# Optimization experiments

Hardware: AMD Instinct MI355X
Metric: run time of the kernel (lower is better)

Reference implementation:

```python
import jax, jax.numpy as jnp
import numpy as np

FEATURE_DIM = 1024
MAX_DEPTH = 32
HID = 128
N = 32768


def setup_inputs() -> dict:
    key = jax.random.key(0)
    ks = jax.random.split(key, 16)
    d = FEATURE_DIM
    s = 0.02
    return {
        "features": jax.random.normal(ks[0], (N, d), jnp.float32),
        "depths": jax.random.randint(ks[1], (N,), 0, MAX_DEPTH),
        "pos_emb": jax.random.normal(ks[2], (MAX_DEPTH, d), jnp.float32) * s,
        "aW1": jax.random.normal(ks[3], (HID, 2 * d), jnp.float32) * s,
        "ab1": jnp.zeros((HID,), jnp.float32),
        "aW2": jax.random.normal(ks[4], (1, HID), jnp.float32) * s,
        "ab2": jnp.zeros((1,), jnp.float32),
        "uW1": jax.random.normal(ks[5], (d, 2 * d), jnp.float32) * s,
        "ub1": jnp.zeros((d,), jnp.float32),
        "uW2": jax.random.normal(ks[6], (d, d), jnp.float32) * s,
        "ub2": jnp.zeros((d,), jnp.float32),
        "gW": jax.random.normal(ks[7], (d, 2 * d), jnp.float32) * s,
        "gb": jnp.zeros((d,), jnp.float32),
    }


def reference(features, depths, pos_emb, aW1, ab1, aW2, ab2,
              uW1, ub1, uW2, ub2, gW, gb):
    # add position embeddings (depths clamped to [0, MAX_DEPTH-1])
    dep = jnp.clip(depths, 0, MAX_DEPTH - 1)
    f = features + pos_emb[dep]                       # [N, d]
    target = f[0:1]                                    # [1, d]
    path = f[1:]                                       # [N-1, d]

    # attention MLP over all path states at once (vectorizes the torch loop)
    tb = jnp.broadcast_to(target, path.shape)          # [N-1, d]
    comb = jnp.concatenate([tb, path], axis=1)         # [N-1, 2d]
    h = jax.nn.relu(comb @ aW1.T + ab1)                # [N-1, 128]
    attn = jax.nn.sigmoid(h @ aW2.T + ab2)             # [N-1, 1]

    s = attn.sum()
    attn = jnp.where(s > 0, attn / s, attn)

    agg = (path * attn).sum(axis=0, keepdims=True)     # [1, d]
    c2 = jnp.concatenate([target, agg], axis=1)        # [1, 2d]
    gate = jax.nn.sigmoid(c2 @ gW.T + gb)
    upd = jax.nn.relu(c2 @ uW1.T + ub1) @ uW2.T + ub2
    updated_target = target + gate * upd
    return jnp.concatenate([updated_target, path], axis=0)
```

## Files before the change

kernel.cpp:

```cpp
#include <hip/hip_runtime.h>

#define DNUM 1024
#define HIDN 128
#define NTOT 32768
#define MR 32
#define NBLK 1024

#define T_OFF 0
#define P0_OFF 1024
#define S_OFF 1152
#define AGG_OFF 1216
#define GATE_OFF 2240
#define U1_OFF 3264
#define W2_FOFF 4288
#define AGGP_OFF (W2_FOFF + 65536)
#define SP_OFF (AGGP_OFF + NBLK * DNUM)
#define WS_NEED ((size_t)(SP_OFF + NBLK) * 4)

typedef __attribute__((ext_vector_type(8))) short short8;
typedef __attribute__((ext_vector_type(4))) float f32x4;

__device__ __forceinline__ unsigned short f2bf(float x) {
  unsigned int u = __builtin_bit_cast(unsigned int, x);
  u = u + 0x7fffu + ((u >> 16) & 1u);
  return (unsigned short)(u >> 16);
}
__device__ __forceinline__ float bf2f(unsigned int bits16) {
  unsigned int u = bits16 << 16;
  return __builtin_bit_cast(float, u);
}

__global__ __launch_bounds__(256) void kinit(const float* __restrict__ features,
                                             const int* __restrict__ depths,
                                             const float* __restrict__ pos_emb,
                                             const float* __restrict__ aW1,
                                             const float* __restrict__ ab1,
                                             float* __restrict__ ws,
                                             unsigned short* __restrict__ w2) {
  int t = threadIdx.x, bid = blockIdx.x;
  if (bid == 0) {
    __shared__ float tgt[1024];
    __shared__ float ph[256];
    int dep = depths[0];
    dep = dep < 0 ? 0 : (dep > 31 ? 31 : dep);
    float4 fv = *(const float4*)(features + t * 4);
    float4 pe = *(const float4*)(pos_emb + dep * DNUM + t * 4);
    float4 r;
    r.x = fv.x + pe.x; r.y = fv.y + pe.y; r.z = fv.z + pe.z; r.w = fv.w + pe.w;
    *(float4*)(ws + T_OFF + t * 4) = r;
    *(float4*)(tgt + t * 4) = r;
    if (t < 64) ws[S_OFF + t] = 0.f;
    __syncthreads();
    int j = t >> 1, h = t & 1;
    const float* wrow = aW1 + (size_t)j * (2 * DNUM) + h * 512;
    const float* tr = tgt + h * 512;
    float p = 0.f;
    for (int k = 0; k < 512; k += 4) {
      float4 wv = *(const float4*)(wrow + k);
      float4 tv = *(const float4*)(tr + k);
      p += wv.x * tv.x + wv.y * tv.y + wv.z * tv.z + wv.w * tv.w;
    }
    ph[t] = p;
    __syncthreads();
    if (t < HIDN) ws[P0_OFF + t] = ab1[t] + ph[t * 2] + ph[t * 2 + 1];
    return;
  }
  int idx = ((bid - 1) * 256 + t) * 4;
  int j = idx >> 10, k = idx & 1023;
  float4 v = *(const float4*)(aW1 + (size_t)j * 2048 + 1024 + k);
  uint2 pk;
  pk.x = (unsigned int)f2bf(v.x) | ((unsigned int)f2bf(v.y) << 16);
  pk.y = (unsigned int)f2bf(v.z) | ((unsigned int)f2bf(v.w) << 16);
  *(uint2*)(w2 + idx) = pk;
}

__global__ __launch_bounds__(256) void kstream(const float* __restrict__ features,
                                               const int* __restrict__ depths,
                                               const float* __restrict__ pos_emb,
                                               float* __restrict__ out) {
  const int t = threadIdx.x;
  const int bid = blockIdx.x;
  const int col = t * 4;
#pragma unroll
  for (int rr = 0; rr < 4; ++rr) {
    int fr = 1 + bid * 4 + rr;
    if (fr < NTOT) {
      int dp = depths[fr];
      dp = dp < 0 ? 0 : (dp > 31 ? 31 : dp);
      float4 fv = *(const float4*)(features + (size_t)fr * DNUM + col);
      float4 pe = *(const float4*)(pos_emb + (size_t)dp * DNUM + col);
      float4 f;
      f.x = fv.x + pe.x; f.y = fv.y + pe.y; f.z = fv.z + pe.z; f.w = fv.w + pe.w;
      *(float4*)(out + (size_t)fr * DNUM + col) = f;
    }
  }
}

__global__ __launch_bounds__(512, 4) void kgemm(
    const float* __restrict__ fsrc, const float* __restrict__ p0,
    const float* __restrict__ aW2, const float* __restrict__ ab2,
    const unsigned short* __restrict__ w2,
    float* __restrict__ agg, float* __restrict__ sacc,
    float* __restrict__ aggp, float* __restrict__ sp) {
  __shared__ __align__(16) unsigned char ldsA[MR * 2048];
  __shared__ float part[160];
  __shared__ float comb[1024];
  const int t = threadIdx.x;
  const int bid = blockIdx.x;
  const int lane = t & 63;
  const int w = t >> 6;
  const int llo = lane & 15;
  const int lhi = lane >> 4;
  const int tc = t & 255;
  const int th = t >> 8;
  const int col = tc * 4;

#pragma unroll
  for (int ii = 0; ii < 16; ++ii) {
    int i = ii * 2 + th;
    int fr = 1 + bid * MR + i;
    float4 f = (fr < NTOT) ? *(const float4*)(fsrc + (size_t)fr * DNUM + col)
                           : make_float4(0.f, 0.f, 0.f, 0.f);
    uint2 pk;
    pk.x = (unsigned int)f2bf(f.x) | ((unsigned int)f2bf(f.y) << 16);
    pk.y = (unsigned int)f2bf(f.z) | ((unsigned int)f2bf(f.w) << 16);
    int off = (i * 2048 + tc * 8) ^ ((i & 7) << 4);
    *(uint2*)(ldsA + off) = pk;
  }
  __syncthreads();

  const int wm = w >> 2, wn = w & 3;
  f32x4 acc[2];
  acc[0] = (f32x4){0.f, 0.f, 0.f, 0.f};
  acc[1] = (f32x4){0.f, 0.f, 0.f, 0.f};
  const int arow = wm * 16 + llo;
  const int abase = arow * 2048;
  const int aswz = (arow & 7) << 4;
  const unsigned short* bpA = w2 + (size_t)(wn * 32 + llo) * DNUM + lhi * 8;
  const unsigned short* bpB = bpA + 16 * DNUM;

#pragma unroll 4
  for (int kc = 0; kc < 32; ++kc) {
    int kbase = kc * 32;
    short8 av = *(short8*)(ldsA + ((abase + (kbase + lhi * 8) * 2) ^ aswz));
    short8 bv0 = *(const short8*)(bpA + kbase);
    short8 bv1 = *(const short8*)(bpB + kbase);
    acc[0] = __builtin_amdgcn_mfma_f32_16x16x32_bf16(av, bv0, acc[0], 0, 0, 0);
    acc[1] = __builtin_amdgcn_mfma_f32_16x16x32_bf16(av, bv1, acc[1], 0, 0, 0);
  }

  float p0v[2], wv[2];
#pragma unroll
  for (int n = 0; n < 2; ++n) {
    int j = wn * 32 + n * 16 + llo;
    p0v[n] = p0[j];
    wv[n] = aW2[j];
  }
#pragma unroll
  for (int e = 0; e < 4; ++e) {
    float s = 0.f;
#pragma unroll
    for (int n = 0; n < 2; ++n) {
      float h = acc[n][e] + p0v[n];
      h = fmaxf(h, 0.f);
      s += h * wv[n];
    }
    s += __shfl_xor(s, 1);
    s += __shfl_xor(s, 2);
    s += __shfl_xor(s, 4);
    s += __shfl_xor(s, 8);
    if (llo == 0) part[wn * 32 + wm * 16 + lhi * 4 + e] = s;
  }
  __syncthreads();

  if (t < MR) {
    float pre = part[t] + part[32 + t] + part[64 + t] + part[96 + t] + ab2[0];
    int fr = 1 + bid * MR + t;
    float raw = 0.f;
    if (fr < NTOT) raw = 1.f / (1.f + __expf(-pre));
    part[128 + t] = raw;
  }
  __syncthreads();

  float a0 = 0.f, a1 = 0.f, a2 = 0.f, a3 = 0.f;
  for (int lr = th * 16; lr < th * 16 + 16; ++lr) {
    float r = part[128 + lr];
    int off = (lr * 2048 + tc * 8) ^ ((lr & 7) << 4);
    uint2 pk = *(uint2*)(ldsA + off);
    a0 += r * bf2f(pk.x & 0xffffu);
    a1 += r * bf2f(pk.x >> 16);
    a2 += r * bf2f(pk.y & 0xffffu);
    a3 += r * bf2f(pk.y >> 16);
  }
  if (th == 1) {
    comb[tc * 4 + 0] = a0; comb[tc * 4 + 1] = a1;
    comb[tc * 4 + 2] = a2; comb[tc * 4 + 3] = a3;
  }
  __syncthreads();
  if (th == 0) {
    float c0 = a0 + comb[tc * 4 + 0];
    float c1 = a1 + comb[tc * 4 + 1];
    float c2v = a2 + comb[tc * 4 + 2];
    float c3 = a3 + comb[tc * 4 + 3];
    if (aggp) {
      f32x4 v = {c0, c1, c2v, c3};
      *(f32x4*)(aggp + (size_t)bid * DNUM + col) = v;
    } else {
      atomicAdd(agg + col + 0, c0);
      atomicAdd(agg + col + 1, c1);
      atomicAdd(agg + col + 2, c2v);
      atomicAdd(agg + col + 3, c3);
    }
  }
  if (t == 0) {
    float s = 0.f;
    for (int lr = 0; lr < MR; ++lr) s += part[128 + lr];
    if (sp) sp[bid] = s;
    else atomicAdd(sacc + (bid & 63), s);
  }
}

__global__ __launch_bounds__(256) void kred(const float* __restrict__ aggp,
                                            const float* __restrict__ sp,
                                            float* __restrict__ ws) {
  int t = threadIdx.x, bid = blockIdx.x;
  if (bid < 256) {
    int w = t >> 6, lane = t & 63;
    int colIdx = bid * 4 + w;
    float s = 0.f;
#pragma unroll 4
    for (int k = 0; k < 16; ++k) {
      int r = lane + k * 64;
      s += aggp[(size_t)r * DNUM + colIdx];
    }
    s += __shfl_xor(s, 1);
    s += __shfl_xor(s, 2);
    s += __shfl_xor(s, 4);
    s += __shfl_xor(s, 8);
    s += __shfl_xor(s, 16);
    s += __shfl_xor(s, 32);
    if (lane == 0) ws[AGG_OFF + colIdx] = s;
  } else {
    __shared__ float red[256];
    float s = sp[t] + sp[t + 256] + sp[t + 512] + sp[t + 768];
    red[t] = s;
    __syncthreads();
    if (t < 64) {
      float v = red[t] + red[t + 64] + red[t + 128] + red[t + 192];
      v += __shfl_xor(v, 1);
      v += __shfl_xor(v, 2);
      v += __shfl_xor(v, 4);
      v += __shfl_xor(v, 8);
      v += __shfl_xor(v, 16);
      v += __shfl_xor(v, 32);
      if (t == 0) ws[S_OFF] = v;
    }
  }
}

__global__ __launch_bounds__(256) void kc1(const float* __restrict__ gW,
                                           const float* __restrict__ gb,
                                           const float* __restrict__ uW1,
                                           const float* __restrict__ ub1,
                                           float* __restrict__ ws) {
  __shared__ float c2[2048];
  __shared__ float sinv_sh;
  int t = threadIdx.x, bid = blockIdx.x;
  if (t == 0) {
    float s = 0.f;
    for (int i = 0; i < 64; ++i) s += ws[S_OFF + i];
    sinv_sh = (s > 0.f) ? 1.f / s : 1.f;
  }
  __syncthreads();
  float sinv = sinv_sh;
  for (int i = t; i < 2048; i += 256)
    c2[i] = (i < 1024) ? ws[T_OFF + i] : ws[AGG_OFF + i - 1024] * sinv;
  __syncthreads();
  int w = t >> 6, lane = t & 63;
  int isGate = bid < 256;
  int o = (isGate ? bid : bid - 256) * 4 + w;
  const float* W = isGate ? gW : uW1;
  float p = 0.f;
  for (int i = lane; i < 2048; i += 64) p += W[(size_t)o * 2048 + i] * c2[i];
  p += __shfl_xor(p, 1);
  p += __shfl_xor(p, 2);
  p += __shfl_xor(p, 4);
  p += __shfl_xor(p, 8);
  p += __shfl_xor(p, 16);
  p += __shfl_xor(p, 32);
  if (lane == 0) {
    float v = p + (isGate ? gb[o] : ub1[o]);
    v = isGate ? (1.f / (1.f + expf(-v))) : fmaxf(v, 0.f);
    ws[(isGate ? GATE_OFF : U1_OFF) + o] = v;
  }
}

__global__ __launch_bounds__(256) void kc2(const float* __restrict__ uW2,
                                           const float* __restrict__ ub2,
                                           const float* __restrict__ ws,
                                           float* __restrict__ out) {
  __shared__ float u1[1024];
  int t = threadIdx.x, bid = blockIdx.x;
  for (int i = t; i < 1024; i += 256) u1[i] = ws[U1_OFF + i];
  __syncthreads();
  int w = t >> 6, lane = t & 63;
  int o = bid * 4 + w;
  float p = 0.f;
  for (int i = lane; i < 1024; i += 64) p += uW2[(size_t)o * 1024 + i] * u1[i];
  p += __shfl_xor(p, 1);
  p += __shfl_xor(p, 2);
  p += __shfl_xor(p, 4);
  p += __shfl_xor(p, 8);
  p += __shfl_xor(p, 16);
  p += __shfl_xor(p, 32);
  if (lane == 0) {
    float upd = p + ub2[o];
    out[o] = ws[T_OFF + o] + ws[GATE_OFF + o] * upd;
  }
}

extern "C" void kernel_launch(void* const* d_in, const int* in_sizes, int n_in,
                              void* d_out, int out_size, void* d_ws, size_t ws_size,
                              hipStream_t stream) {
  const float* features = (const float*)d_in[0];
  const int* depths = (const int*)d_in[1];
  const float* pos_emb = (const float*)d_in[2];
  const float* aW1 = (const float*)d_in[3];
  const float* ab1 = (const float*)d_in[4];
  const float* aW2 = (const float*)d_in[5];
  const float* ab2 = (const float*)d_in[6];
  const float* uW1 = (const float*)d_in[7];
  const float* ub1 = (const float*)d_in[8];
  const float* uW2 = (const float*)d_in[9];
  const float* ub2 = (const float*)d_in[10];
  const float* gW = (const float*)d_in[11];
  const float* gb = (const float*)d_in[12];
  float* out = (float*)d_out;
  float* ws = (float*)d_ws;
  unsigned short* w2 = (unsigned short*)(ws + W2_FOFF);
  bool useP = ws_size >= WS_NEED;
  float* aggp = useP ? (ws + AGGP_OFF) : nullptr;
  float* sp = useP ? (ws + SP_OFF) : nullptr;

  hipLaunchKernelGGL(kinit, dim3(129), dim3(256), 0, stream,
                     features, depths, pos_emb, aW1, ab1, ws, w2);
  hipLaunchKernelGGL(kstream, dim3(8192), dim3(256), 0, stream,
                     features, depths, pos_emb, out);
  hipLaunchKernelGGL(kgemm, dim3(NBLK), dim3(512), 0, stream,
                     out, ws + P0_OFF, aW2, ab2, w2, ws + AGG_OFF, ws + S_OFF, aggp, sp);
  if (useP)
    hipLaunchKernelGGL(kred, dim3(257), dim3(256), 0, stream, aggp, sp, ws);
  hipLaunchKernelGGL(kc1, dim3(512), dim3(256), 0, stream, gW, gb, uW1, ub1, ws);
  hipLaunchKernelGGL(kc2, dim3(256), dim3(256), 0, stream, uW2, ub2, ws, out);
}
```

Baseline: 179.9 us.

## Fuse init into stream kernel and prestage swizzled bf16 path tiles for GEMM

Merges the init and streaming kernels into one launch, and has the streaming pass also write a pre-swizzled bf16 copy of each 32-row path tile into workspace. The GEMM kernel then fills its LDS tile with direct global-to-LDS loads of that copy instead of re-reading fp32 rows and converting them. This halves the bytes the GEMM reads for its A operand and removes one launch. In exchange the streaming pass writes an extra 64 MB, and the fast path only runs when the workspace is large enough.

```diff
diff --git a/kernel.cpp b/kernel.cpp
--- a/kernel.cpp
+++ b/kernel.cpp
@@ -5,6 +5,7 @@
 #define NTOT 32768
 #define MR 32
 #define NBLK 1024
+#define SBLK 8192
 
 #define T_OFF 0
 #define P0_OFF 1024
@@ -16,6 +17,8 @@
 #define AGGP_OFF (W2_FOFF + 65536)
 #define SP_OFF (AGGP_OFF + NBLK * DNUM)
 #define WS_NEED ((size_t)(SP_OFF + NBLK) * 4)
+#define FBF_BYTE ((((SP_OFF + NBLK) * 4) + 65535) & ~65535)
+#define WS_NEED2 ((size_t)FBF_BYTE + (size_t)NBLK * 65536)
 
 typedef __attribute__((ext_vector_type(8))) short short8;
 typedef __attribute__((ext_vector_type(4))) float f32x4;
@@ -29,18 +32,52 @@
   unsigned int u = bits16 << 16;
   return __builtin_bit_cast(float, u);
 }
-
-__global__ __launch_bounds__(256) void kinit(const float* __restrict__ features,
-                                             const int* __restrict__ depths,
-                                             const float* __restrict__ pos_emb,
-                                             const float* __restrict__ aW1,
-                                             const float* __restrict__ ab1,
-                                             float* __restrict__ ws,
-                                             unsigned short* __restrict__ w2) {
-  int t = threadIdx.x, bid = blockIdx.x;
-  if (bid == 0) {
-    __shared__ float tgt[1024];
-    __shared__ float ph[256];
+__device__ __forceinline__ void gl_lds16(const void* g, void* l) {
+  __builtin_amdgcn_global_load_lds(
+      (const __attribute__((address_space(1))) unsigned int*)g,
+      (__attribute__((address_space(3))) unsigned int*)l, 16, 0, 0);
+}
+
+__global__ __launch_bounds__(256) void kf1(const float* __restrict__ features,
+                                           const int* __restrict__ depths,
+                                           const float* __restrict__ pos_emb,
+                                           const float* __restrict__ aW1,
+                                           const float* __restrict__ ab1,
+                                           float* __restrict__ ws,
+                                           unsigned short* __restrict__ w2,
+                                           float* __restrict__ out,
+                                           unsigned short* __restrict__ fbf) {
+  __shared__ float tgt[1024];
+  __shared__ float ph[256];
+  const int t = threadIdx.x;
+  const int bid = blockIdx.x;
+  if (bid < SBLK) {
+    const int col = t * 4;
+#pragma unroll
+    for (int rr = 0; rr < 4; ++rr) {
+      int fr = 1 + bid * 4 + rr;
+      float4 f = make_float4(0.f, 0.f, 0.f, 0.f);
+      if (fr < NTOT) {
+        int dp = depths[fr];
+        dp = dp < 0 ? 0 : (dp > 31 ? 31 : dp);
+        float4 fv = *(const float4*)(features + (size_t)fr * DNUM + col);
+        float4 pe = *(const float4*)(pos_emb + (size_t)dp * DNUM + col);
+        f.x = fv.x + pe.x; f.y = fv.y + pe.y; f.z = fv.z + pe.z; f.w = fv.w + pe.w;
+        *(float4*)(out + (size_t)fr * DNUM + col) = f;
+      }
+      if (fbf) {
+        uint2 pk;
+        pk.x = (unsigned int)f2bf(f.x) | ((unsigned int)f2bf(f.y) << 16);
+        pk.y = (unsigned int)f2bf(f.z) | ((unsigned int)f2bf(f.w) << 16);
+        int g = (fr - 1) >> 5, i = (fr - 1) & 31;
+        int off = (i * 2048 + t * 8) ^ ((i & 7) << 4);
+        *(uint2*)((char*)fbf + (size_t)g * 65536 + off) = pk;
+      }
+    }
+    return;
+  }
+  int ib = bid - SBLK;
+  if (ib == 0) {
     int dep = depths[0];
     dep = dep < 0 ? 0 : (dep > 31 ? 31 : dep);
     float4 fv = *(const float4*)(features + t * 4);
@@ -65,7 +102,7 @@
     if (t < HIDN) ws[P0_OFF + t] = ab1[t] + ph[t * 2] + ph[t * 2 + 1];
     return;
   }
-  int idx = ((bid - 1) * 256 + t) * 4;
+  int idx = ((ib - 1) * 256 + t) * 4;
   int j = idx >> 10, k = idx & 1023;
   float4 v = *(const float4*)(aW1 + (size_t)j * 2048 + 1024 + k);
   uint2 pk;
@@ -74,34 +111,13 @@
   *(uint2*)(w2 + idx) = pk;
 }
 
-__global__ __launch_bounds__(256) void kstream(const float* __restrict__ features,
-                                               const int* __restrict__ depths,
-                                               const float* __restrict__ pos_emb,
-                                               float* __restrict__ out) {
-  const int t = threadIdx.x;
-  const int bid = blockIdx.x;
-  const int col = t * 4;
-#pragma unroll
-  for (int rr = 0; rr < 4; ++rr) {
-    int fr = 1 + bid * 4 + rr;
-    if (fr < NTOT) {
-      int dp = depths[fr];
-      dp = dp < 0 ? 0 : (dp > 31 ? 31 : dp);
-      float4 fv = *(const float4*)(features + (size_t)fr * DNUM + col);
-      float4 pe = *(const float4*)(pos_emb + (size_t)dp * DNUM + col);
-      float4 f;
-      f.x = fv.x + pe.x; f.y = fv.y + pe.y; f.z = fv.z + pe.z; f.w = fv.w + pe.w;
-      *(float4*)(out + (size_t)fr * DNUM + col) = f;
-    }
-  }
-}
-
 __global__ __launch_bounds__(512, 4) void kgemm(
     const float* __restrict__ fsrc, const float* __restrict__ p0,
     const float* __restrict__ aW2, const float* __restrict__ ab2,
     const unsigned short* __restrict__ w2,
     float* __restrict__ agg, float* __restrict__ sacc,
-    float* __restrict__ aggp, float* __restrict__ sp) {
+    float* __restrict__ aggp, float* __restrict__ sp,
+    const unsigned short* __restrict__ fbf) {
   __shared__ __align__(16) unsigned char ldsA[MR * 2048];
   __shared__ float part[160];
   __shared__ float comb[1024];
@@ -115,17 +131,27 @@
   const int th = t >> 8;
   const int col = tc * 4;
 
-#pragma unroll
-  for (int ii = 0; ii < 16; ++ii) {
-    int i = ii * 2 + th;
-    int fr = 1 + bid * MR + i;
-    float4 f = (fr < NTOT) ? *(const float4*)(fsrc + (size_t)fr * DNUM + col)
-                           : make_float4(0.f, 0.f, 0.f, 0.f);
-    uint2 pk;
-    pk.x = (unsigned int)f2bf(f.x) | ((unsigned int)f2bf(f.y) << 16);
-    pk.y = (unsigned int)f2bf(f.z) | ((unsigned int)f2bf(f.w) << 16);
-    int off = (i * 2048 + tc * 8) ^ ((i & 7) << 4);
-    *(uint2*)(ldsA + off) = pk;
+  if (fbf) {
+    const char* src = (const char*)fbf + (size_t)bid * 65536;
+#pragma unroll
+    for (int q = 0; q < 8; ++q) {
+      int wb = q * 8192 + w * 1024;
+      gl_lds16(src + wb + lane * 16, ldsA + wb);
+    }
+    asm volatile("s_waitcnt vmcnt(0)" ::: "memory");
+  } else {
+#pragma unroll
+    for (int ii = 0; ii < 16; ++ii) {
+      int i = ii * 2 + th;
+      int fr = 1 + bid * MR + i;
+      float4 f = (fr < NTOT) ? *(const float4*)(fsrc + (size_t)fr * DNUM + col)
+                             : make_float4(0.f, 0.f, 0.f, 0.f);
+      uint2 pk;
+      pk.x = (unsigned int)f2bf(f.x) | ((unsigned int)f2bf(f.y) << 16);
+      pk.y = (unsigned int)f2bf(f.z) | ((unsigned int)f2bf(f.w) << 16);
+      int off = (i * 2048 + tc * 8) ^ ((i & 7) << 4);
+      *(uint2*)(ldsA + off) = pk;
+    }
   }
   __syncthreads();
 
@@ -339,15 +365,16 @@
   float* ws = (float*)d_ws;
   unsigned short* w2 = (unsigned short*)(ws + W2_FOFF);
   bool useP = ws_size >= WS_NEED;
+  bool useF = ws_size >= WS_NEED2;
   float* aggp = useP ? (ws + AGGP_OFF) : nullptr;
   float* sp = useP ? (ws + SP_OFF) : nullptr;
-
-  hipLaunchKernelGGL(kinit, dim3(129), dim3(256), 0, stream,
-                     features, depths, pos_emb, aW1, ab1, ws, w2);
-  hipLaunchKernelGGL(kstream, dim3(8192), dim3(256), 0, stream,
-                     features, depths, pos_emb, out);
+  unsigned short* fbf = useF ? (unsigned short*)((char*)d_ws + FBF_BYTE) : nullptr;
+
+  hipLaunchKernelGGL(kf1, dim3(SBLK + 129), dim3(256), 0, stream,
+                     features, depths, pos_emb, aW1, ab1, ws, w2, out, fbf);
   hipLaunchKernelGGL(kgemm, dim3(NBLK), dim3(512), 0, stream,
-                     out, ws + P0_OFF, aW2, ab2, w2, ws + AGG_OFF, ws + S_OFF, aggp, sp);
+                     out, ws + P0_OFF, aW2, ab2, w2, ws + AGG_OFF, ws + S_OFF,
+                     aggp, sp, fbf);
   if (useP)
     hipLaunchKernelGGL(kred, dim3(257), dim3(256), 0, stream, aggp, sp, ws);
   hipLaunchKernelGGL(kc1, dim3(512), dim3(256), 0, stream, gW, gb, uW1, ub1, ws);
```

Result: no change. 181.3 us (+0.8%).

## Fuse position-embedding stream pass into attention GEMM kernel with smaller row tiles

Applied to the files above, without the earlier changes.

Removes the separate kstream kernel and has the GEMM kernel compute features+pos_emb itself, writing the output rows and packing bf16 tiles directly. This drops one full write-then-read of the 128MB activation through HBM. Tiles shrink to 16 rows with 256-thread blocks across 2048 blocks, which removes the cross-half combine step. The cost is more per-block partial aggregates for kred to reduce. kinit now also zeroes the agg buffer.

```diff
diff --git a/kernel.cpp b/kernel.cpp
--- a/kernel.cpp
+++ b/kernel.cpp
@@ -3,8 +3,8 @@
 #define DNUM 1024
 #define HIDN 128
 #define NTOT 32768
-#define MR 32
-#define NBLK 1024
+#define MR 16
+#define NBLK 2048
 
 #define T_OFF 0
 #define P0_OFF 1024
@@ -37,10 +37,10 @@
                                              const float* __restrict__ ab1,
                                              float* __restrict__ ws,
                                              unsigned short* __restrict__ w2) {
+  __shared__ float tgt[1024];
+  __shared__ float ph[256];
   int t = threadIdx.x, bid = blockIdx.x;
   if (bid == 0) {
-    __shared__ float tgt[1024];
-    __shared__ float ph[256];
     int dep = depths[0];
     dep = dep < 0 ? 0 : (dep > 31 ? 31 : dep);
     float4 fv = *(const float4*)(features + t * 4);
@@ -49,6 +49,8 @@
     r.x = fv.x + pe.x; r.y = fv.y + pe.y; r.z = fv.z + pe.z; r.w = fv.w + pe.w;
     *(float4*)(ws + T_OFF + t * 4) = r;
     *(float4*)(tgt + t * 4) = r;
+    float4 z = make_float4(0.f, 0.f, 0.f, 0.f);
+    *(float4*)(ws + AGG_OFF + t * 4) = z;
     if (t < 64) ws[S_OFF + t] = 0.f;
     __syncthreads();
     int j = t >> 1, h = t & 1;
@@ -74,69 +76,48 @@
   *(uint2*)(w2 + idx) = pk;
 }
 
-__global__ __launch_bounds__(256) void kstream(const float* __restrict__ features,
-                                               const int* __restrict__ depths,
-                                               const float* __restrict__ pos_emb,
-                                               float* __restrict__ out) {
-  const int t = threadIdx.x;
-  const int bid = blockIdx.x;
-  const int col = t * 4;
-#pragma unroll
-  for (int rr = 0; rr < 4; ++rr) {
-    int fr = 1 + bid * 4 + rr;
-    if (fr < NTOT) {
-      int dp = depths[fr];
-      dp = dp < 0 ? 0 : (dp > 31 ? 31 : dp);
-      float4 fv = *(const float4*)(features + (size_t)fr * DNUM + col);
-      float4 pe = *(const float4*)(pos_emb + (size_t)dp * DNUM + col);
-      float4 f;
-      f.x = fv.x + pe.x; f.y = fv.y + pe.y; f.z = fv.z + pe.z; f.w = fv.w + pe.w;
-      *(float4*)(out + (size_t)fr * DNUM + col) = f;
-    }
-  }
-}
-
-__global__ __launch_bounds__(512, 4) void kgemm(
-    const float* __restrict__ fsrc, const float* __restrict__ p0,
+__global__ __launch_bounds__(256, 4) void kbig(
+    const float* __restrict__ features, const int* __restrict__ depths,
+    const float* __restrict__ pos_emb, const float* __restrict__ p0,
     const float* __restrict__ aW2, const float* __restrict__ ab2,
-    const unsigned short* __restrict__ w2,
+    const unsigned short* __restrict__ w2, float* __restrict__ out,
     float* __restrict__ agg, float* __restrict__ sacc,
     float* __restrict__ aggp, float* __restrict__ sp) {
   __shared__ __align__(16) unsigned char ldsA[MR * 2048];
-  __shared__ float part[160];
-  __shared__ float comb[1024];
+  __shared__ float part[80];
   const int t = threadIdx.x;
   const int bid = blockIdx.x;
   const int lane = t & 63;
   const int w = t >> 6;
   const int llo = lane & 15;
   const int lhi = lane >> 4;
-  const int tc = t & 255;
-  const int th = t >> 8;
-  const int col = tc * 4;
-
-#pragma unroll
-  for (int ii = 0; ii < 16; ++ii) {
-    int i = ii * 2 + th;
+  const int col = t * 4;
+
+  for (int i = 0; i < MR; ++i) {
     int fr = 1 + bid * MR + i;
-    float4 f = (fr < NTOT) ? *(const float4*)(fsrc + (size_t)fr * DNUM + col)
-                           : make_float4(0.f, 0.f, 0.f, 0.f);
+    float4 f = make_float4(0.f, 0.f, 0.f, 0.f);
+    if (fr < NTOT) {
+      int dp = depths[fr];
+      dp = dp < 0 ? 0 : (dp > 31 ? 31 : dp);
+      float4 fv = *(const float4*)(features + (size_t)fr * DNUM + col);
+      float4 pe = *(const float4*)(pos_emb + (size_t)dp * DNUM + col);
+      f.x = fv.x + pe.x; f.y = fv.y + pe.y; f.z = fv.z + pe.z; f.w = fv.w + pe.w;
+      *(float4*)(out + (size_t)fr * DNUM + col) = f;
+    }
     uint2 pk;
     pk.x = (unsigned int)f2bf(f.x) | ((unsigned int)f2bf(f.y) << 16);
     pk.y = (unsigned int)f2bf(f.z) | ((unsigned int)f2bf(f.w) << 16);
-    int off = (i * 2048 + tc * 8) ^ ((i & 7) << 4);
+    int off = (i * 2048 + t * 8) ^ ((i & 7) << 4);
     *(uint2*)(ldsA + off) = pk;
   }
   __syncthreads();
 
-  const int wm = w >> 2, wn = w & 3;
   f32x4 acc[2];
   acc[0] = (f32x4){0.f, 0.f, 0.f, 0.f};
   acc[1] = (f32x4){0.f, 0.f, 0.f, 0.f};
-  const int arow = wm * 16 + llo;
-  const int abase = arow * 2048;
-  const int aswz = (arow & 7) << 4;
-  const unsigned short* bpA = w2 + (size_t)(wn * 32 + llo) * DNUM + lhi * 8;
+  const int abase = llo * 2048;
+  const int aswz = (llo & 7) << 4;
+  const unsigned short* bpA = w2 + (size_t)(w * 32 + llo) * DNUM + lhi * 8;
   const unsigned short* bpB = bpA + 16 * DNUM;
 
 #pragma unroll 4
@@ -152,7 +133,7 @@
   float p0v[2], wv[2];
 #pragma unroll
   for (int n = 0; n < 2; ++n) {
-    int j = wn * 32 + n * 16 + llo;
+    int j = w * 32 + n * 16 + llo;
     p0v[n] = p0[j];
     wv[n] = aW2[j];
   }
@@ -169,52 +150,42 @@
     s += __shfl_xor(s, 2);
     s += __shfl_xor(s, 4);
     s += __shfl_xor(s, 8);
-    if (llo == 0) part[wn * 32 + wm * 16 + lhi * 4 + e] = s;
+    if (llo == 0) part[w * 16 + lhi * 4 + e] = s;
   }
   __syncthreads();
 
   if (t < MR) {
-    float pre = part[t] + part[32 + t] + part[64 + t] + part[96 + t] + ab2[0];
+    float pre = part[t] + part[16 + t] + part[32 + t] + part[48 + t] + ab2[0];
     int fr = 1 + bid * MR + t;
     float raw = 0.f;
     if (fr < NTOT) raw = 1.f / (1.f + __expf(-pre));
-    part[128 + t] = raw;
+    part[64 + t] = raw;
   }
   __syncthreads();
 
   float a0 = 0.f, a1 = 0.f, a2 = 0.f, a3 = 0.f;
-  for (int lr = th * 16; lr < th * 16 + 16; ++lr) {
-    float r = part[128 + lr];
-    int off = (lr * 2048 + tc * 8) ^ ((lr & 7) << 4);
+#pragma unroll
+  for (int lr = 0; lr < MR; ++lr) {
+    float r = part[64 + lr];
+    int off = (lr * 2048 + t * 8) ^ ((lr & 7) << 4);
     uint2 pk = *(uint2*)(ldsA + off);
     a0 += r * bf2f(pk.x & 0xffffu);
     a1 += r * bf2f(pk.x >> 16);
     a2 += r * bf2f(pk.y & 0xffffu);
     a3 += r * bf2f(pk.y >> 16);
   }
-  if (th == 1) {
-    comb[tc * 4 + 0] = a0; comb[tc * 4 + 1] = a1;
-    comb[tc * 4 + 2] = a2; comb[tc * 4 + 3] = a3;
-  }
-  __syncthreads();
-  if (th == 0) {
-    float c0 = a0 + comb[tc * 4 + 0];
-    float c1 = a1 + comb[tc * 4 + 1];
-    float c2v = a2 + comb[tc * 4 + 2];
-    float c3 = a3 + comb[tc * 4 + 3];
-    if (aggp) {
-      f32x4 v = {c0, c1, c2v, c3};
-      *(f32x4*)(aggp + (size_t)bid * DNUM + col) = v;
-    } else {
-      atomicAdd(agg + col + 0, c0);
-      atomicAdd(agg + col + 1, c1);
-      atomicAdd(agg + col + 2, c2v);
-      atomicAdd(agg + col + 3, c3);
-    }
+  if (aggp) {
+    f32x4 v = {a0, a1, a2, a3};
+    *(f32x4*)(aggp + (size_t)bid * DNUM + col) = v;
+  } else {
+    atomicAdd(agg + col + 0, a0);
+    atomicAdd(agg + col + 1, a1);
+    atomicAdd(agg + col + 2, a2);
+    atomicAdd(agg + col + 3, a3);
   }
   if (t == 0) {
     float s = 0.f;
-    for (int lr = 0; lr < MR; ++lr) s += part[128 + lr];
+    for (int lr = 0; lr < MR; ++lr) s += part[64 + lr];
     if (sp) sp[bid] = s;
     else atomicAdd(sacc + (bid & 63), s);
   }
@@ -229,7 +200,7 @@
     int colIdx = bid * 4 + w;
     float s = 0.f;
 #pragma unroll 4
-    for (int k = 0; k < 16; ++k) {
+    for (int k = 0; k < NBLK / 64; ++k) {
       int r = lane + k * 64;
       s += aggp[(size_t)r * DNUM + colIdx];
     }
@@ -242,7 +213,8 @@
     if (lane == 0) ws[AGG_OFF + colIdx] = s;
   } else {
     __shared__ float red[256];
-    float s = sp[t] + sp[t + 256] + sp[t + 512] + sp[t + 768];
+    float s = 0.f;
+    for (int k = t; k < NBLK; k += 256) s += sp[k];
     red[t] = s;
     __syncthreads();
     if (t < 64) {
@@ -344,10 +316,9 @@
 
   hipLaunchKernelGGL(kinit, dim3(129), dim3(256), 0, stream,
                      features, depths, pos_emb, aW1, ab1, ws, w2);
-  hipLaunchKernelGGL(kstream, dim3(8192), dim3(256), 0, stream,
-                     features, depths, pos_emb, out);
-  hipLaunchKernelGGL(kgemm, dim3(NBLK), dim3(512), 0, stream,
-                     out, ws + P0_OFF, aW2, ab2, w2, ws + AGG_OFF, ws + S_OFF, aggp, sp);
+  hipLaunchKernelGGL(kbig, dim3(NBLK), dim3(256), 0, stream,
+                     features, depths, pos_emb, ws + P0_OFF, aW2, ab2, w2, out,
+                     ws + AGG_OFF, ws + S_OFF, aggp, sp);
   if (useP)
     hipLaunchKernelGGL(kred, dim3(257), dim3(256), 0, stream, aggp, sp, ws);
   hipLaunchKernelGGL(kc1, dim3(512), dim3(256), 0, stream, gW, gb, uW1, ub1, ws);
```

After: 176.1 us. 2.1% less time.

## Fuse stream copy into GEMM kernel with interleaved heterogeneous blocks

Applied to the files above, without the earlier changes.

Merges the separate path-copy kernel and the attention GEMM kernel into one launch. Every fifth block runs the GEMM tile and reads features plus pos_emb directly instead of rereading the written output. The other four blocks in each group write the output copy. This removes a kernel boundary and the dependent read of the output buffer, so copy traffic can overlap GEMM compute. In exchange the GEMM blocks redo the pos_emb add, and the launch_bounds occupancy hint is dropped.

```diff
diff --git a/kernel.cpp b/kernel.cpp
--- a/kernel.cpp
+++ b/kernel.cpp
@@ -5,6 +5,8 @@
 #define NTOT 32768
 #define MR 32
 #define NBLK 1024
+#define NGRP 1024
+#define TOTB (NGRP * 5)
 
 #define T_OFF 0
 #define P0_OFF 1024
@@ -37,10 +39,10 @@
                                              const float* __restrict__ ab1,
                                              float* __restrict__ ws,
                                              unsigned short* __restrict__ w2) {
+  __shared__ float tgt[1024];
+  __shared__ float ph[256];
   int t = threadIdx.x, bid = blockIdx.x;
   if (bid == 0) {
-    __shared__ float tgt[1024];
-    __shared__ float ph[256];
     int dep = depths[0];
     dep = dep < 0 ? 0 : (dep > 31 ? 31 : dep);
     float4 fv = *(const float4*)(features + t * 4);
@@ -49,6 +51,8 @@
     r.x = fv.x + pe.x; r.y = fv.y + pe.y; r.z = fv.z + pe.z; r.w = fv.w + pe.w;
     *(float4*)(ws + T_OFF + t * 4) = r;
     *(float4*)(tgt + t * 4) = r;
+    float4 z = make_float4(0.f, 0.f, 0.f, 0.f);
+    *(float4*)(ws + AGG_OFF + t * 4) = z;
     if (t < 64) ws[S_OFF + t] = 0.f;
     __syncthreads();
     int j = t >> 1, h = t & 1;
@@ -74,53 +78,61 @@
   *(uint2*)(w2 + idx) = pk;
 }
 
-__global__ __launch_bounds__(256) void kstream(const float* __restrict__ features,
-                                               const int* __restrict__ depths,
-                                               const float* __restrict__ pos_emb,
-                                               float* __restrict__ out) {
-  const int t = threadIdx.x;
-  const int bid = blockIdx.x;
-  const int col = t * 4;
-#pragma unroll
-  for (int rr = 0; rr < 4; ++rr) {
-    int fr = 1 + bid * 4 + rr;
-    if (fr < NTOT) {
-      int dp = depths[fr];
-      dp = dp < 0 ? 0 : (dp > 31 ? 31 : dp);
-      float4 fv = *(const float4*)(features + (size_t)fr * DNUM + col);
-      float4 pe = *(const float4*)(pos_emb + (size_t)dp * DNUM + col);
-      float4 f;
-      f.x = fv.x + pe.x; f.y = fv.y + pe.y; f.z = fv.z + pe.z; f.w = fv.w + pe.w;
-      *(float4*)(out + (size_t)fr * DNUM + col) = f;
-    }
-  }
-}
-
-__global__ __launch_bounds__(512, 4) void kgemm(
-    const float* __restrict__ fsrc, const float* __restrict__ p0,
+__global__ __launch_bounds__(512) void kmain(
+    const float* __restrict__ features, const int* __restrict__ depths,
+    const float* __restrict__ pos_emb, const float* __restrict__ p0,
     const float* __restrict__ aW2, const float* __restrict__ ab2,
-    const unsigned short* __restrict__ w2,
+    const unsigned short* __restrict__ w2, float* __restrict__ out,
     float* __restrict__ agg, float* __restrict__ sacc,
     float* __restrict__ aggp, float* __restrict__ sp) {
   __shared__ __align__(16) unsigned char ldsA[MR * 2048];
   __shared__ float part[160];
   __shared__ float comb[1024];
   const int t = threadIdx.x;
-  const int bid = blockIdx.x;
+  const int b = blockIdx.x;
+  const int q = b / 5;
+  const int r5 = b - q * 5;
+  const int tc = t & 255;
+  const int th = t >> 8;
+  const int col = tc * 4;
+
+  if (r5 != 0) {
+    const int s = q * 4 + (r5 - 1);
+#pragma unroll
+    for (int iter = 0; iter < 4; ++iter) {
+      int i = iter * 2 + th;
+      int fr = 1 + s * 8 + i;
+      if (fr < NTOT) {
+        int dp = depths[fr];
+        dp = dp < 0 ? 0 : (dp > 31 ? 31 : dp);
+        float4 fv = *(const float4*)(features + (size_t)fr * DNUM + col);
+        float4 pe = *(const float4*)(pos_emb + (size_t)dp * DNUM + col);
+        float4 f;
+        f.x = fv.x + pe.x; f.y = fv.y + pe.y; f.z = fv.z + pe.z; f.w = fv.w + pe.w;
+        *(float4*)(out + (size_t)fr * DNUM + col) = f;
+      }
+    }
+    return;
+  }
+
+  const int bid = q;
   const int lane = t & 63;
   const int w = t >> 6;
   const int llo = lane & 15;
   const int lhi = lane >> 4;
-  const int tc = t & 255;
-  const int th = t >> 8;
-  const int col = tc * 4;
 
 #pragma unroll
   for (int ii = 0; ii < 16; ++ii) {
     int i = ii * 2 + th;
     int fr = 1 + bid * MR + i;
-    float4 f = (fr < NTOT) ? *(const float4*)(fsrc + (size_t)fr * DNUM + col)
-                           : make_float4(0.f, 0.f, 0.f, 0.f);
+    float4 f = make_float4(0.f, 0.f, 0.f, 0.f);
+    if (fr < NTOT) {
+      int dp = depths[fr];
+      dp = dp < 0 ? 0 : (dp > 31 ? 31 : dp);
+      float4 fv = *(const float4*)(features + (size_t)fr * DNUM + col);
+      float4 pe = *(const float4*)(pos_emb + (size_t)dp * DNUM + col);
+      f.x = fv.x + pe.x; f.y = fv.y + pe.y; f.z = fv.z + pe.z; f.w = fv.w + pe.w;
+    }
     uint2 pk;
     pk.x = (unsigned int)f2bf(f.x) | ((unsigned int)f2bf(f.y) << 16);
     pk.y = (unsigned int)f2bf(f.z) | ((unsigned int)f2bf(f.w) << 16);
@@ -229,7 +241,7 @@
     int colIdx = bid * 4 + w;
     float s = 0.f;
 #pragma unroll 4
-    for (int k = 0; k < 16; ++k) {
+    for (int k = 0; k < NBLK / 64; ++k) {
       int r = lane + k * 64;
       s += aggp[(size_t)r * DNUM + colIdx];
     }
@@ -242,7 +254,8 @@
     if (lane == 0) ws[AGG_OFF + colIdx] = s;
   } else {
     __shared__ float red[256];
-    float s = sp[t] + sp[t + 256] + sp[t + 512] + sp[t + 768];
+    float s = 0.f;
+    for (int k = t; k < NBLK; k += 256) s += sp[k];
     red[t] = s;
     __syncthreads();
     if (t < 64) {
@@ -344,10 +357,9 @@
 
   hipLaunchKernelGGL(kinit, dim3(129), dim3(256), 0, stream,
                      features, depths, pos_emb, aW1, ab1, ws, w2);
-  hipLaunchKernelGGL(kstream, dim3(8192), dim3(256), 0, stream,
-                     features, depths, pos_emb, out);
-  hipLaunchKernelGGL(kgemm, dim3(NBLK), dim3(512), 0, stream,
-                     out, ws + P0_OFF, aW2, ab2, w2, ws + AGG_OFF, ws + S_OFF, aggp, sp);
+  hipLaunchKernelGGL(kmain, dim3(TOTB), dim3(512), 0, stream,
+                     features, depths, pos_emb, ws + P0_OFF, aW2, ab2, w2, out,
+                     ws + AGG_OFF, ws + S_OFF, aggp, sp);
   if (useP)
     hipLaunchKernelGGL(kred, dim3(257), dim3(256), 0, stream, aggp, sp, ws);
   hipLaunchKernelGGL(kc1, dim3(512), dim3(256), 0, stream, gW, gb, uW1, ub1, ws);
```

After: 190.2 us. 1.06x slower.
